# Kernel tuning notes

Measured on AMD Instinct MI355X. Metric: run time of the kernel, lower is better.

## Reference

```python
import jax, jax.numpy as jnp
import numpy as np

NEG_BIG = -9e15
ALPHA = 0.2  # LeakyReLU negative slope


def setup_inputs() -> dict:
    key = jax.random.key(0)
    k1, k2, k3, k4 = jax.random.split(key, 4)
    N, Fin, Fout = 8192, 256, 256
    input_ = jax.random.normal(k1, (N, Fin), dtype=jnp.float32)
    adj = jax.random.randint(k2, (N, N), 0, 2, dtype=jnp.int32)
    # xavier_uniform with gain=1.414
    limW = 1.414 * np.sqrt(6.0 / (Fin + Fout))
    W = jax.random.uniform(k3, (Fin, Fout), minval=-limW, maxval=limW, dtype=jnp.float32)
    lima = 1.414 * np.sqrt(6.0 / (2 * Fout + 1))
    a = jax.random.uniform(k4, (2 * Fout, 1), minval=-lima, maxval=lima, dtype=jnp.float32)
    return {"input_": input_, "adj": adj, "W": W, "a": a}


def reference(input_, adj, W, a):
    # h: [N, F]
    h = input_ @ W
    F = h.shape[1]
    # Decompose cat([h_i, h_j]) @ a into per-node projections summed by broadcast
    src = h @ a[:F, 0]   # [N]  contribution of row node i
    dst = h @ a[F:, 0]   # [N]  contribution of col node j
    e = jax.nn.leaky_relu(src[:, None] + dst[None, :], negative_slope=ALPHA)  # [N, N]
    e = jnp.where(adj > 0, e, NEG_BIG)
    attention = jax.nn.softmax(e, axis=1)
    h_prime = attention @ h  # [N, F]
    return jax.nn.relu(h_prime)  # concat=True
```

## Files before the change

### kernel.cpp

```cpp
#include <hip/hip_runtime.h>
#include <math.h>

#define NN 8192
#define FF 256
#define ALPHA 0.2f
#define SS 4
#define JSEG (NN / SS)
#define STEPS (JSEG / 32)

typedef __bf16 bf16x8 __attribute__((ext_vector_type(8)));
typedef __bf16 bf16x4 __attribute__((ext_vector_type(4)));
typedef float  f32x4  __attribute__((ext_vector_type(4)));

__device__ __forceinline__ void dma16(const void* g, void* l) {
    __builtin_amdgcn_global_load_lds((const __attribute__((address_space(1))) void*)g,
                                     (__attribute__((address_space(3))) void*)l,
                                     16, 0, 0);
}

#define VMCNT4   asm volatile("s_waitcnt vmcnt(4)" ::: "memory")
#define LGKM0    asm volatile("s_waitcnt lgkmcnt(0)" ::: "memory")
#define BARRIER  asm volatile("s_barrier" ::: "memory")
#define FENCE    asm volatile("" ::: "memory")

__global__ __launch_bounds__(256) void k0_wt(const float* __restrict__ W,
                                             __bf16* __restrict__ WT) {
    __shared__ float ts[64][65];
    const int t = threadIdx.x;
    const int k0 = blockIdx.x * 64;
    const int n0 = blockIdx.y * 64;
    #pragma unroll
    for (int r = 0; r < 4; ++r) {
        int krow = r * 16 + (t >> 4);
        int nc4 = (t & 15) * 4;
        *(float4*)&ts[krow][nc4] = *(const float4*)&W[(size_t)(k0 + krow) * FF + n0 + nc4];
    }
    __syncthreads();
    const int nloc = t >> 2;
    const int kc = (t & 3) * 16;
    union { bf16x8 v[2]; __bf16 e[16]; } hi, lo;
    #pragma unroll
    for (int u = 0; u < 16; ++u) {
        float x = ts[kc + u][nloc];
        __bf16 h1 = (__bf16)x;
        hi.e[u] = h1;
        lo.e[u] = (__bf16)(x - (float)h1);
    }
    size_t base = (size_t)(n0 + nloc) * FF + k0 + kc;
    *(bf16x8*)&WT[base] = hi.v[0];
    *(bf16x8*)&WT[base + 8] = hi.v[1];
    size_t lbase = (size_t)FF * FF + base;
    *(bf16x8*)&WT[lbase] = lo.v[0];
    *(bf16x8*)&WT[lbase + 8] = lo.v[1];
}

__global__ __launch_bounds__(256) void k1_h(const float* __restrict__ X,
                                            const __bf16* __restrict__ WT,
                                            const float* __restrict__ a,
                                            __bf16* __restrict__ hT,
                                            float* __restrict__ src,
                                            float* __restrict__ dst) {
    __shared__ __bf16 ax[2][32][40];
    __shared__ float hs[32][264];
    __shared__ float red[2][4][32];
    const int t = threadIdx.x;
    const int i0 = blockIdx.x * 32;
    const int l = t & 63, wv = t >> 6, ln = l & 15, g = l >> 4;
    f32x4 acc[2][4];
    #pragma unroll
    for (int mt = 0; mt < 2; ++mt)
        #pragma unroll
        for (int nt = 0; nt < 4; ++nt)
            acc[mt][nt] = (f32x4){0.f, 0.f, 0.f, 0.f};

    for (int ks = 0; ks < 8; ++ks) {
        const int k0 = ks * 32;
        {
            int row = t >> 3, c4 = (t & 7) * 4;
            float4 xv = *(const float4*)&X[(size_t)(i0 + row) * FF + k0 + c4];
            bf16x4 hi4, lo4;
            float xs_[4] = {xv.x, xv.y, xv.z, xv.w};
            #pragma unroll
            for (int u = 0; u < 4; ++u) {
                __bf16 h1 = (__bf16)xs_[u];
                hi4[u] = h1;
                lo4[u] = (__bf16)(xs_[u] - (float)h1);
            }
            *(bf16x4*)&ax[0][row][c4] = hi4;
            *(bf16x4*)&ax[1][row][c4] = lo4;
        }
        __syncthreads();
        bf16x8 ah[2], al[2];
        ah[0] = *(bf16x8*)&ax[0][ln][g * 8];
        ah[1] = *(bf16x8*)&ax[0][16 + ln][g * 8];
        al[0] = *(bf16x8*)&ax[1][ln][g * 8];
        al[1] = *(bf16x8*)&ax[1][16 + ln][g * 8];
        #pragma unroll
        for (int nt = 0; nt < 4; ++nt) {
            const int n = wv * 64 + nt * 16 + ln;
            bf16x8 bh8 = *(const bf16x8*)&WT[(size_t)n * FF + k0 + g * 8];
            bf16x8 bl8 = *(const bf16x8*)&WT[(size_t)(FF + n) * FF + k0 + g * 8];
            #pragma unroll
            for (int mt = 0; mt < 2; ++mt) {
                acc[mt][nt] = __builtin_amdgcn_mfma_f32_16x16x32_bf16(ah[mt], bh8, acc[mt][nt], 0, 0, 0);
                acc[mt][nt] = __builtin_amdgcn_mfma_f32_16x16x32_bf16(ah[mt], bl8, acc[mt][nt], 0, 0, 0);
                acc[mt][nt] = __builtin_amdgcn_mfma_f32_16x16x32_bf16(al[mt], bh8, acc[mt][nt], 0, 0, 0);
            }
        }
        __syncthreads();
    }
    float an[4], ad[4];
    #pragma unroll
    for (int nt = 0; nt < 4; ++nt) {
        an[nt] = a[wv * 64 + nt * 16 + ln];
        ad[nt] = a[FF + wv * 64 + nt * 16 + ln];
    }
    float sp[2][4], dp[2][4];
    #pragma unroll
    for (int mt = 0; mt < 2; ++mt)
        #pragma unroll
        for (int rg = 0; rg < 4; ++rg) { sp[mt][rg] = 0.f; dp[mt][rg] = 0.f; }
    #pragma unroll
    for (int mt = 0; mt < 2; ++mt)
        #pragma unroll
        for (int nt = 0; nt < 4; ++nt)
            #pragma unroll
            for (int rg = 0; rg < 4; ++rg) {
                float v = acc[mt][nt][rg];
                hs[mt * 16 + g * 4 + rg][wv * 64 + nt * 16 + ln] = v;
                sp[mt][rg] += v * an[nt];
                dp[mt][rg] += v * ad[nt];
            }
    #pragma unroll
    for (int mk = 1; mk < 16; mk <<= 1)
        #pragma unroll
        for (int mt = 0; mt < 2; ++mt)
            #pragma unroll
            for (int rg = 0; rg < 4; ++rg) {
                sp[mt][rg] += __shfl_xor(sp[mt][rg], mk);
                dp[mt][rg] += __shfl_xor(dp[mt][rg], mk);
            }
    if (ln == 0) {
        #pragma unroll
        for (int mt = 0; mt < 2; ++mt)
            #pragma unroll
            for (int rg = 0; rg < 4; ++rg) {
                red[0][wv][mt * 16 + g * 4 + rg] = sp[mt][rg];
                red[1][wv][mt * 16 + g * 4 + rg] = dp[mt][rg];
            }
    }
    __syncthreads();
    if (t < 32) {
        src[i0 + t] = red[0][0][t] + red[0][1][t] + red[0][2][t] + red[0][3][t];
        dst[i0 + t] = red[1][0][t] + red[1][1][t] + red[1][2][t] + red[1][3][t];
    }
    {
        const int f = t;
        #pragma unroll
        for (int jc = 0; jc < 4; ++jc) {
            union { bf16x8 v; __bf16 e[8]; } hi, lo;
            #pragma unroll
            for (int u = 0; u < 8; ++u) {
                float x = hs[jc * 8 + u][f];
                __bf16 h1 = (__bf16)x;
                hi.e[u] = h1;
                lo.e[u] = (__bf16)(x - (float)h1);
            }
            *(bf16x8*)&hT[(size_t)f * NN + i0 + jc * 8] = hi.v;
            *(bf16x8*)&hT[(size_t)(FF + f) * NN + i0 + jc * 8] = lo.v;
        }
    }
}

__global__ __launch_bounds__(256) void k2b_max(const float* __restrict__ dst,
                                               float* __restrict__ maxd) {
    __shared__ float red[256];
    float m = -1e30f;
    #pragma unroll
    for (int r = 0; r < NN / 1024; ++r) {
        float4 v = *(const float4*)&dst[(r * 256 + threadIdx.x) * 4];
        m = fmaxf(m, fmaxf(fmaxf(v.x, v.y), fmaxf(v.z, v.w)));
    }
    red[threadIdx.x] = m;
    __syncthreads();
    for (int s = 128; s > 0; s >>= 1) {
        if (threadIdx.x < s) red[threadIdx.x] = fmaxf(red[threadIdx.x], red[threadIdx.x + s]);
        __syncthreads();
    }
    if (threadIdx.x == 0) maxd[0] = red[0];
}

__global__ __launch_bounds__(256, 2) void k3_attn(const int* __restrict__ adj,
                                                  const __bf16* __restrict__ hT,
                                                  const float* __restrict__ src,
                                                  const float* __restrict__ dst,
                                                  const float* __restrict__ maxd,
                                                  float* __restrict__ num,
                                                  float* __restrict__ den) {
    __shared__ __bf16 bh[2][2048 * 8];
    __shared__ __bf16 wA[2][64][40];
    __shared__ float dl[64][4];
    const int t = threadIdx.x;
    const int l = t & 63, wv = t >> 6, ln = l & 15, g = l >> 4;
    const int it = blockIdx.x & 127;
    const int seg = blockIdx.x >> 7;
    const int i0 = it * 64;
    const int jbeg = seg * JSEG;
    const int p_i = t >> 2, p_q = t & 3;
    const float maxdv = maxd[0];
    const float src_r = src[i0 + p_i];
    const float e0 = src_r + maxdv;
    const float m_r = e0 > 0.f ? e0 : ALPHA * e0;

    int rowbase[8], cb[8];
    #pragma unroll
    for (int r = 0; r < 8; ++r) {
        int cbase = r * 256 + wv * 64;
        int c = cbase + l;
        int hl = c >> 10;
        int f = (c >> 2) & 255;
        int pc = c & 3;
        int jc = pc ^ ((f >> 1) & 3);
        rowbase[r] = (hl * FF + f) * NN + jc * 8;
        cb[r] = __builtin_amdgcn_readfirstlane(cbase);
    }
    const int* arow = adj + (size_t)(i0 + p_i) * NN + p_q * 8;
    const float* drow = dst + p_q * 8;

    int4 a0e, a1e, a0o, a1o;
    float4 d0e, d1e, d0o, d1o;

    a0e = *(const int4*)(arow + jbeg);
    a1e = *(const int4*)(arow + jbeg + 4);
    d0e = *(const float4*)(drow + jbeg);
    d1e = *(const float4*)(drow + jbeg + 4);
    FENCE;
    #pragma unroll
    for (int r = 0; r < 8; ++r)
        dma16(&hT[rowbase[r] + jbeg], &bh[0][cb[r] * 8]);
    FENCE;
    a0o = *(const int4*)(arow + jbeg + 32);
    a1o = *(const int4*)(arow + jbeg + 32 + 4);
    d0o = *(const float4*)(drow + jbeg + 32);
    d1o = *(const float4*)(drow + jbeg + 32 + 4);
    FENCE;

    float den_reg = 0.f;
    f32x4 acc[4][4];
    #pragma unroll
    for (int mt = 0; mt < 4; ++mt)
        #pragma unroll
        for (int nt = 0; nt < 4; ++nt)
            acc[mt][nt] = (f32x4){0.f, 0.f, 0.f, 0.f};

#define K3_WCOMP(A0_, A1_, D0_, D1_, P_)                                      \
    {                                                                         \
        const int av[8] = {A0_.x, A0_.y, A0_.z, A0_.w,                        \
                           A1_.x, A1_.y, A1_.z, A1_.w};                       \
        const float dv[8] = {D0_.x, D0_.y, D0_.z, D0_.w,                      \
                             D1_.x, D1_.y, D1_.z, D1_.w};                     \
        union { bf16x8 v; __bf16 e[8]; } wu;                                  \
        _Pragma("unroll")                                                     \
        for (int u = 0; u < 8; ++u) {                                         \
            float e = src_r + dv[u];                                          \
            e = e > 0.f ? e : ALPHA * e;                                      \
            float w = (av[u] > 0) ? __expf(e - m_r) : 0.f;                    \
            den_reg += w;                                                     \
            wu.e[u] = (__bf16)w;                                              \
        }                                                                     \
        *(bf16x8*)&wA[P_][p_i][p_q * 8] = wu.v;                               \
    }

#define K3_PREF(A0_, A1_, D0_, D1_, JN_)                                      \
    A0_ = *(const int4*)(arow + (JN_));                                       \
    A1_ = *(const int4*)(arow + (JN_) + 4);                                   \
    D0_ = *(const float4*)(drow + (JN_));                                     \
    D1_ = *(const float4*)(drow + (JN_) + 4);

#define K3_DMA(J1_, P_)                                                       \
    {                                                                         \
        _Pragma("unroll")                                                     \
        for (int r = 0; r < 8; ++r)                                           \
            dma16(&hT[rowbase[r] + (J1_)], &bh[P_][cb[r] * 8]);               \
    }

#define K3_MFMA(P_)                                                           \
    {                                                                         \
        bf16x8 af[4];                                                         \
        _Pragma("unroll")                                                     \
        for (int mt = 0; mt < 4; ++mt)                                        \
            af[mt] = *(bf16x8*)&wA[P_][mt * 16 + ln][g * 8];                  \
        _Pragma("unroll")                                                     \
        for (int nt = 0; nt < 4; ++nt) {                                      \
            const int f = wv * 64 + nt * 16 + ln;                             \
            const int sw = (f >> 1) & 3;                                      \
            _Pragma("unroll")                                                 \
            for (int hl = 0; hl < 2; ++hl) {                                  \
                const int chunk = (hl * FF + f) * 4 + (g ^ sw);               \
                bf16x8 bfr = *(bf16x8*)&bh[P_][chunk * 8];                    \
                _Pragma("unroll")                                             \
                for (int mt = 0; mt < 4; ++mt)                                \
                    acc[mt][nt] = __builtin_amdgcn_mfma_f32_16x16x32_bf16(    \
                        af[mt], bfr, acc[mt][nt], 0, 0, 0);                   \
            }                                                                 \
        }                                                                     \
    }

    for (int su = 0; su < STEPS; su += 2) {
        K3_WCOMP(a0e, a1e, d0e, d1e, 0);
        {
            const int jn = (su + 2 < STEPS) ? jbeg + (su + 2) * 32 : jbeg;
            K3_PREF(a0e, a1e, d0e, d1e, jn);
        }
        FENCE; VMCNT4; LGKM0; BARRIER;
        K3_DMA(jbeg + (su + 1) * 32, 1);
        FENCE;
        K3_MFMA(0);
        K3_WCOMP(a0o, a1o, d0o, d1o, 1);
        {
            const int jn = (su + 3 < STEPS) ? jbeg + (su + 3) * 32 : jbeg;
            K3_PREF(a0o, a1o, d0o, d1o, jn);
        }
        FENCE; VMCNT4; LGKM0; BARRIER;
        {
            const int j2 = (su + 2 < STEPS) ? jbeg + (su + 2) * 32 : jbeg;
            K3_DMA(j2, 0);
        }
        FENCE;
        K3_MFMA(1);
    }
    __syncthreads();
    #pragma unroll
    for (int mt = 0; mt < 4; ++mt)
        #pragma unroll
        for (int nt = 0; nt < 4; ++nt)
            #pragma unroll
            for (int rg = 0; rg < 4; ++rg)
                num[((size_t)seg * NN + i0 + mt * 16 + g * 4 + rg) * FF
                    + wv * 64 + nt * 16 + ln] = acc[mt][nt][rg];
    dl[p_i][p_q] = den_reg;
    __syncthreads();
    if (t < 64) den[(size_t)seg * NN + i0 + t] = dl[t][0] + dl[t][1] + dl[t][2] + dl[t][3];
}

__global__ __launch_bounds__(256) void k4_out(const float* __restrict__ num,
                                              const float* __restrict__ den,
                                              float* __restrict__ out) {
    size_t f4 = (size_t)blockIdx.x * 256 + threadIdx.x;
    int i = (int)(f4 >> 6);
    int c4 = (int)(f4 & 63) << 2;
    float4 s = make_float4(0.f, 0.f, 0.f, 0.f);
    float d = 0.f;
    #pragma unroll
    for (int sg = 0; sg < SS; ++sg) {
        float4 v = *(const float4*)&num[((size_t)sg * NN + i) * FF + c4];
        s.x += v.x; s.y += v.y; s.z += v.z; s.w += v.w;
        d += den[(size_t)sg * NN + i];
    }
    float inv = 1.f / d;
    float4 o;
    o.x = fmaxf(s.x * inv, 0.f);
    o.y = fmaxf(s.y * inv, 0.f);
    o.z = fmaxf(s.z * inv, 0.f);
    o.w = fmaxf(s.w * inv, 0.f);
    *(float4*)&out[(size_t)i * FF + c4] = o;
}

extern "C" void kernel_launch(void* const* d_in, const int* in_sizes, int n_in,
                              void* d_out, int out_size, void* d_ws, size_t ws_size,
                              hipStream_t stream) {
    const float* X  = (const float*)d_in[0];
    const int*  adj = (const int*)d_in[1];
    const float* W  = (const float*)d_in[2];
    const float* a  = (const float*)d_in[3];
    float* out = (float*)d_out;
    char* ws = (char*)d_ws;

    const size_t off_hT   = 0;
    const size_t off_wt   = off_hT + (size_t)2 * FF * NN * 2;
    const size_t off_src  = off_wt + (size_t)2 * FF * FF * 2;
    const size_t off_dst  = off_src + (size_t)NN * 4;
    const size_t off_maxd = off_dst + (size_t)NN * 4;
    const size_t off_num  = off_maxd + 256;
    const size_t off_den  = off_num + (size_t)SS * NN * FF * 4;

    __bf16* hT_ws = (__bf16*)(ws + off_hT);
    __bf16* wt_ws = (__bf16*)(ws + off_wt);
    float* src_ws = (float*)(ws + off_src);
    float* dst_ws = (float*)(ws + off_dst);
    float* maxd   = (float*)(ws + off_maxd);
    float* num_ws = (float*)(ws + off_num);
    float* den_ws = (float*)(ws + off_den);

    k0_wt<<<dim3(FF / 64, FF / 64), 256, 0, stream>>>(W, wt_ws);
    k1_h<<<NN / 32, 256, 0, stream>>>(X, wt_ws, a, hT_ws, src_ws, dst_ws);
    k2b_max<<<1, 256, 0, stream>>>(dst_ws, maxd);
    k3_attn<<<(NN / 64) * SS, 256, 0, stream>>>(adj, hT_ws, src_ws, dst_ws, maxd,
                                                num_ws, den_ws);
    k4_out<<<(NN * FF / 4) / 256, 256, 0, stream>>>(num_ws, den_ws, out);
}
```

Before: 486.0 us.

## Remap attention waves to own 16 rows and build weight fragments in registers

Each wave now owns 16 output rows across all 256 features instead of 64 features across 64 rows. The softmax weights are built directly in registers as the MFMA A operand, which removes the shared wA staging buffer and its store/load round trip. The low-half bf16 component of h is no longer loaded or multiplied, so LDS traffic and the MFMA count are halved, at some cost in accuracy. The den reduction now uses lane shuffles instead of shared memory, and with the smaller LDS footprint the launch bound rises to 3 blocks per CU.

Result: faster. 463.7 us (-4.6%).

```diff
diff --git a/kernel.cpp b/kernel.cpp
--- a/kernel.cpp
+++ b/kernel.cpp
@@ -190,42 +190,43 @@
     if (threadIdx.x == 0) maxd[0] = red[0];
 }
 
-__global__ __launch_bounds__(256, 2) void k3_attn(const int* __restrict__ adj,
+__global__ __launch_bounds__(256, 3) void k3_attn(const int* __restrict__ adj,
                                                   const __bf16* __restrict__ hT,
                                                   const float* __restrict__ src,
                                                   const float* __restrict__ dst,
                                                   const float* __restrict__ maxd,
                                                   float* __restrict__ num,
                                                   float* __restrict__ den) {
-    __shared__ __bf16 bh[2][2048 * 8];
-    __shared__ __bf16 wA[2][64][40];
-    __shared__ float dl[64][4];
+    __shared__ __bf16 bh[2][1024 * 8];
     const int t = threadIdx.x;
     const int l = t & 63, wv = t >> 6, ln = l & 15, g = l >> 4;
     const int it = blockIdx.x & 127;
     const int seg = blockIdx.x >> 7;
     const int i0 = it * 64;
     const int jbeg = seg * JSEG;
-    const int p_i = t >> 2, p_q = t & 3;
+    const int row = i0 + wv * 16 + ln;
     const float maxdv = maxd[0];
-    const float src_r = src[i0 + p_i];
+    const float src_r = src[row];
     const float e0 = src_r + maxdv;
     const float m_r = e0 > 0.f ? e0 : ALPHA * e0;
 
-    int rowbase[8], cb[8];
-    #pragma unroll
-    for (int r = 0; r < 8; ++r) {
+    int ga[4], cb[4];
+    #pragma unroll
+    for (int r = 0; r < 4; ++r) {
         int cbase = r * 256 + wv * 64;
         int c = cbase + l;
-        int hl = c >> 10;
-        int f = (c >> 2) & 255;
+        int f = c >> 2;
         int pc = c & 3;
         int jc = pc ^ ((f >> 1) & 3);
-        rowbase[r] = (hl * FF + f) * NN + jc * 8;
+        ga[r] = f * NN + jc * 8;
         cb[r] = __builtin_amdgcn_readfirstlane(cbase);
     }
-    const int* arow = adj + (size_t)(i0 + p_i) * NN + p_q * 8;
-    const float* drow = dst + p_q * 8;
+    const int* arow = adj + (size_t)row * NN + g * 8;
+    const float* drow = dst + g * 8;
+
+    const int rb = ln * 64 + ((g ^ ((ln >> 1) & 3)) * 16);
+    const char* bh0 = (const char*)&bh[0][0] + rb;
+    const char* bh1 = (const char*)&bh[1][0] + rb;
 
     int4 a0e, a1e, a0o, a1o;
     float4 d0e, d1e, d0o, d1o;
@@ -236,8 +237,8 @@
     d1e = *(const float4*)(drow + jbeg + 4);
     FENCE;
     #pragma unroll
-    for (int r = 0; r < 8; ++r)
-        dma16(&hT[rowbase[r] + jbeg], &bh[0][cb[r] * 8]);
+    for (int r = 0; r < 4; ++r)
+        dma16(&hT[ga[r] + jbeg], &bh[0][cb[r] * 8]);
     FENCE;
     a0o = *(const int4*)(arow + jbeg + 32);
     a1o = *(const int4*)(arow + jbeg + 32 + 4);
@@ -246,29 +247,24 @@
     FENCE;
 
     float den_reg = 0.f;
-    f32x4 acc[4][4];
-    #pragma unroll
-    for (int mt = 0; mt < 4; ++mt)
-        #pragma unroll
-        for (int nt = 0; nt < 4; ++nt)
-            acc[mt][nt] = (f32x4){0.f, 0.f, 0.f, 0.f};
-
-#define K3_WCOMP(A0_, A1_, D0_, D1_, P_)                                      \
+    f32x4 acc[16];
+    #pragma unroll
+    for (int nt = 0; nt < 16; ++nt) acc[nt] = (f32x4){0.f, 0.f, 0.f, 0.f};
+
+#define K3_WCOMP(A0_, A1_, D0_, D1_, AF_)                                     \
     {                                                                         \
         const int av[8] = {A0_.x, A0_.y, A0_.z, A0_.w,                        \
                            A1_.x, A1_.y, A1_.z, A1_.w};                       \
         const float dv[8] = {D0_.x, D0_.y, D0_.z, D0_.w,                      \
                              D1_.x, D1_.y, D1_.z, D1_.w};                     \
-        union { bf16x8 v; __bf16 e[8]; } wu;                                  \
         _Pragma("unroll")                                                     \
         for (int u = 0; u < 8; ++u) {                                         \
             float e = src_r + dv[u];                                          \
             e = e > 0.f ? e : ALPHA * e;                                      \
             float w = (av[u] > 0) ? __expf(e - m_r) : 0.f;                    \
             den_reg += w;                                                     \
-            wu.e[u] = (__bf16)w;                                              \
+            AF_[u] = (__bf16)w;                                               \
         }                                                                     \
-        *(bf16x8*)&wA[P_][p_i][p_q * 8] = wu.v;                               \
     }
 
 #define K3_PREF(A0_, A1_, D0_, D1_, JN_)                                      \
@@ -280,34 +276,23 @@
 #define K3_DMA(J1_, P_)                                                       \
     {                                                                         \
         _Pragma("unroll")                                                     \
-        for (int r = 0; r < 8; ++r)                                           \
-            dma16(&hT[rowbase[r] + (J1_)], &bh[P_][cb[r] * 8]);               \
-    }
-
-#define K3_MFMA(P_)                                                           \
+        for (int r = 0; r < 4; ++r)                                           \
+            dma16(&hT[ga[r] + (J1_)], &bh[P_][cb[r] * 8]);                    \
+    }
+
+#define K3_MFMA(AF_, BP_)                                                     \
     {                                                                         \
-        bf16x8 af[4];                                                         \
         _Pragma("unroll")                                                     \
-        for (int mt = 0; mt < 4; ++mt)                                        \
-            af[mt] = *(bf16x8*)&wA[P_][mt * 16 + ln][g * 8];                  \
-        _Pragma("unroll")                                                     \
-        for (int nt = 0; nt < 4; ++nt) {                                      \
-            const int f = wv * 64 + nt * 16 + ln;                             \
-            const int sw = (f >> 1) & 3;                                      \
-            _Pragma("unroll")                                                 \
-            for (int hl = 0; hl < 2; ++hl) {                                  \
-                const int chunk = (hl * FF + f) * 4 + (g ^ sw);               \
-                bf16x8 bfr = *(bf16x8*)&bh[P_][chunk * 8];                    \
-                _Pragma("unroll")                                             \
-                for (int mt = 0; mt < 4; ++mt)                                \
-                    acc[mt][nt] = __builtin_amdgcn_mfma_f32_16x16x32_bf16(    \
-                        af[mt], bfr, acc[mt][nt], 0, 0, 0);                   \
-            }                                                                 \
+        for (int nt = 0; nt < 16; ++nt) {                                     \
+            bf16x8 bfr = *(const bf16x8*)((BP_) + nt * 1024);                 \
+            acc[nt] = __builtin_amdgcn_mfma_f32_16x16x32_bf16(                \
+                AF_, bfr, acc[nt], 0, 0, 0);                                  \
         }                                                                     \
     }
 
     for (int su = 0; su < STEPS; su += 2) {
-        K3_WCOMP(a0e, a1e, d0e, d1e, 0);
+        bf16x8 afe;
+        K3_WCOMP(a0e, a1e, d0e, d1e, afe);
         {
             const int jn = (su + 2 < STEPS) ? jbeg + (su + 2) * 32 : jbeg;
             K3_PREF(a0e, a1e, d0e, d1e, jn);
@@ -315,8 +300,9 @@
         FENCE; VMCNT4; LGKM0; BARRIER;
         K3_DMA(jbeg + (su + 1) * 32, 1);
         FENCE;
-        K3_MFMA(0);
-        K3_WCOMP(a0o, a1o, d0o, d1o, 1);
+        K3_MFMA(afe, bh0);
+        bf16x8 afo;
+        K3_WCOMP(a0o, a1o, d0o, d1o, afo);
         {
             const int jn = (su + 3 < STEPS) ? jbeg + (su + 3) * 32 : jbeg;
             K3_PREF(a0o, a1o, d0o, d1o, jn);
@@ -327,20 +313,17 @@
             K3_DMA(j2, 0);
         }
         FENCE;
-        K3_MFMA(1);
-    }
-    __syncthreads();
-    #pragma unroll
-    for (int mt = 0; mt < 4; ++mt)
-        #pragma unroll
-        for (int nt = 0; nt < 4; ++nt)
-            #pragma unroll
-            for (int rg = 0; rg < 4; ++rg)
-                num[((size_t)seg * NN + i0 + mt * 16 + g * 4 + rg) * FF
-                    + wv * 64 + nt * 16 + ln] = acc[mt][nt][rg];
-    dl[p_i][p_q] = den_reg;
-    __syncthreads();
-    if (t < 64) den[(size_t)seg * NN + i0 + t] = dl[t][0] + dl[t][1] + dl[t][2] + dl[t][3];
+        K3_MFMA(afo, bh1);
+    }
+    den_reg += __shfl_xor(den_reg, 16);
+    den_reg += __shfl_xor(den_reg, 32);
+    if (g == 0) den[(size_t)seg * NN + row] = den_reg;
+    #pragma unroll
+    for (int nt = 0; nt < 16; ++nt)
+        #pragma unroll
+        for (int rg = 0; rg < 4; ++rg)
+            num[((size_t)seg * NN + i0 + wv * 16 + g * 4 + rg) * FF
+                + nt * 16 + ln] = acc[nt][rg];
 }
 
 __global__ __launch_bounds__(256) void k4_out(const float* __restrict__ num,
```
